# Kernel tuning notes

Hardware: AMD Instinct MI355X
Metric: run time of the kernel (lower is better)

## Reference

```python
import jax, jax.numpy as jnp
import numpy as np

B, C, H, Wd = 4, 64, 64, 64


def setup_inputs() -> dict:
    key = jax.random.key(0)
    k1, k2, k3 = jax.random.split(key, 3)
    x = jax.random.normal(k1, (B, C, H, Wd), dtype=jnp.float32)
    W = jax.random.normal(k2, (C, C), dtype=jnp.float32) * (1.0 / np.sqrt(C))
    b = jax.random.normal(k3, (C,), dtype=jnp.float32) * 0.01
    return {"x": x, "W": W, "b": b}


def reference(x, W, b):
    Bz, Cz, Hz, Wz = x.shape
    N = Hz * Wz
    xf = x.reshape(Bz, Cz, N)                      # values [B,C,N]
    # shared 1x1 conv for queries and keys (same module instance in torch)
    qk = jnp.einsum('oc,bcn->bon', W, xf) + b[None, :, None]  # [B,C,N]
    # scores[b,n,m] = sum_c q[b,c,n] * k[b,c,m], scaled by 1/N
    scores = jnp.einsum('bcn,bcm->bnm', qk, qk) / N           # [B,N,N]
    attn = jax.nn.softmax(scores, axis=-1)                    # softmax over m
    # out[b,c,n] = sum_m values[b,c,m] * attn[b,n,m]
    out = jnp.einsum('bcm,bnm->bcn', xf, attn)
    return out.reshape(Bz, Cz, Hz, Wz)
```

## Files before the change

kernel.cpp:

```cpp
#include <hip/hip_runtime.h>
#include <hip/hip_bf16.h>

#define BATCH 4
#define NSP   4096

#define QKSCALE 0.0187675376f

typedef __bf16 bf16x8v __attribute__((ext_vector_type(8)));
typedef __bf16 bf16x4v __attribute__((ext_vector_type(4)));
typedef float  floatx4 __attribute__((ext_vector_type(4)));
typedef float  floatx16 __attribute__((ext_vector_type(16)));
typedef unsigned uivec2 __attribute__((ext_vector_type(2)));

static __device__ __forceinline__ float fast_exp2(float x) {
#if __has_builtin(__builtin_amdgcn_exp2f)
    return __builtin_amdgcn_exp2f(x);
#else
    return exp2f(x);
#endif
}

static __device__ __forceinline__ unsigned pkbf(float a, float b) {
    union { __bf16 h[2]; unsigned u; } x;
    x.h[0] = (__bf16)a; x.h[1] = (__bf16)b;
    return x.u;
}

static __device__ __forceinline__ void plswap(unsigned &a, unsigned &b) {
#if __has_builtin(__builtin_amdgcn_permlane32_swap)
    uivec2 r = __builtin_amdgcn_permlane32_swap(a, b, false, false);
    a = r[0]; b = r[1];
#else
    asm("v_permlane32_swap_b32 %0, %1" : "+v"(a), "+v"(b));
#endif
}

__global__ __launch_bounds__(256) void qk_kernel(const float* __restrict__ x,
                                                 const float* __restrict__ Wm,
                                                 const float* __restrict__ bias,
                                                 __bf16* __restrict__ qkT,
                                                 __bf16* __restrict__ xbf) {
    __shared__ __align__(16) __bf16 xT[64 * 72];

    const int t  = threadIdx.x;
    const int b  = blockIdx.x >> 6;
    const int n0 = (blockIdx.x & 63) << 6;

#pragma unroll
    for (int p = 0; p < 4; ++p) {
        const int c  = p * 16 + (t >> 4);
        const int n4 = (t & 15) * 4;
        const float4 v = *(const float4*)(x + (size_t)(b * 64 + c) * 4096 + n0 + n4);
        xT[(n4 + 0) * 72 + c] = (__bf16)(v.x * QKSCALE);
        xT[(n4 + 1) * 72 + c] = (__bf16)(v.y * QKSCALE);
        xT[(n4 + 2) * 72 + c] = (__bf16)(v.z * QKSCALE);
        xT[(n4 + 3) * 72 + c] = (__bf16)(v.w * QKSCALE);
        bf16x4v xv;
        xv[0] = (__bf16)v.x; xv[1] = (__bf16)v.y; xv[2] = (__bf16)v.z; xv[3] = (__bf16)v.w;
        *(bf16x4v*)(xbf + (size_t)(b * 64 + c) * 4096 + n0 + n4) = xv;
    }
    __syncthreads();

    const int w = t >> 6, lane = t & 63, quad = lane >> 4, l16 = lane & 15;
    const bf16x8v a0 = *(const bf16x8v*)(xT + (w * 16 + l16) * 72 + quad * 8);
    const bf16x8v a1 = *(const bf16x8v*)(xT + (w * 16 + l16) * 72 + 32 + quad * 8);

    floatx4 acc[4];
#pragma unroll
    for (int ot = 0; ot < 4; ++ot) {
        const float* wr = Wm + (ot * 16 + l16) * 64;
        float4 wa = *(const float4*)(wr + quad * 8);
        float4 wb = *(const float4*)(wr + quad * 8 + 4);
        float4 wc = *(const float4*)(wr + 32 + quad * 8);
        float4 wd = *(const float4*)(wr + 32 + quad * 8 + 4);
        bf16x8v b0, b1;
        b0[0]=(__bf16)wa.x; b0[1]=(__bf16)wa.y; b0[2]=(__bf16)wa.z; b0[3]=(__bf16)wa.w;
        b0[4]=(__bf16)wb.x; b0[5]=(__bf16)wb.y; b0[6]=(__bf16)wb.z; b0[7]=(__bf16)wb.w;
        b1[0]=(__bf16)wc.x; b1[1]=(__bf16)wc.y; b1[2]=(__bf16)wc.z; b1[3]=(__bf16)wc.w;
        b1[4]=(__bf16)wd.x; b1[5]=(__bf16)wd.y; b1[6]=(__bf16)wd.z; b1[7]=(__bf16)wd.w;
        acc[ot] = floatx4{0.f, 0.f, 0.f, 0.f};
        acc[ot] = __builtin_amdgcn_mfma_f32_16x16x32_bf16(a0, b0, acc[ot], 0, 0, 0);
        acc[ot] = __builtin_amdgcn_mfma_f32_16x16x32_bf16(a1, b1, acc[ot], 0, 0, 0);
    }
    __syncthreads();

#pragma unroll
    for (int ot = 0; ot < 4; ++ot) {
        const float bo = bias[ot * 16 + l16] * QKSCALE;
#pragma unroll
        for (int r = 0; r < 4; ++r)
            xT[(w * 16 + quad * 4 + r) * 72 + ot * 16 + l16] = (__bf16)(acc[ot][r] + bo);
    }
    __syncthreads();

    const int n = t >> 2, seg = t & 3;
    __bf16* dst = qkT + (size_t)(b * 4096 + n0 + n) * 64 + seg * 16;
    *(bf16x8v*)dst       = *(const bf16x8v*)(xT + n * 72 + seg * 16);
    *(bf16x8v*)(dst + 8) = *(const bf16x8v*)(xT + n * 72 + seg * 16 + 8);
}

template<int SPLIT, int ITERS>
__global__ __launch_bounds__(512, 4) void attn_kernel(const __bf16* __restrict__ xbf,
                                                      const __bf16* __restrict__ qkT,
                                                      __bf16* __restrict__ Opart,
                                                      float* __restrict__ Lpart) {
    __shared__ __align__(16) char smem[66560];
    __bf16* Klds = (__bf16*)smem;
    __bf16* Vlds = (__bf16*)(smem + 16384);
    float*  Olds = (float*)smem;

    const int t   = threadIdx.x;
    const int blk = blockIdx.x;
    const int xcd = blk & 7;
    const int b   = xcd >> 1;
    const int sub = ((blk >> 3) << 1) | (xcd & 1);
    const int qt  = sub / SPLIT;
    const int s   = sub % SPLIT;
    const int n0  = qt << 8;
    const int pblk = (b * 16 + qt) * SPLIT + s;

    const int w = t >> 6, lane = t & 63, l31 = lane & 31, hi = lane >> 5;

    const __bf16* kgl = qkT + (size_t)b * 4096 * 64;
    const __bf16* vgl = xbf + (size_t)b * 64 * 4096;

    bf16x8v qf[4];
    {
        const __bf16* qrow = kgl + (size_t)(n0 + w * 32 + l31) * 64;
#pragma unroll
        for (int kb = 0; kb < 4; ++kb)
            qf[kb] = *(const bf16x8v*)(qrow + kb * 16 + hi * 8);
    }

    floatx16 oacc[2] = {};
    float rs = 0.f;

    const int srow = t >> 3;
    const int scol = t & 7;
    const int slot = ((scol ^ (srow & 7)) * 8);
    uint4 kst, vst;
    auto stage_load = [&](int m0) {
        kst = *(const uint4*)(kgl + (size_t)(m0 + srow) * 64 + scol * 8);
        vst = *(const uint4*)(vgl + (size_t)srow * 4096 + m0 + scol * 8);
    };
    auto stage_write = [&](int buf) {
        *(uint4*)(Klds + buf * 4096 + srow * 64 + slot) = kst;
        *(uint4*)(Vlds + buf * 4096 + srow * 64 + slot) = vst;
    };

    const int mbase = s * (64 * ITERS);
    stage_load(mbase);
    stage_write(0);
    int cur = 0;

    for (int it = 0; it < ITERS; ++it) {
        if (it + 1 < ITERS) stage_load(mbase + ((it + 1) << 6));
        __syncthreads();
        const __bf16* Kc = Klds + cur * 4096;
        const __bf16* Vc = Vlds + cur * 4096;

        __builtin_amdgcn_s_setprio(1);
#pragma unroll
        for (int mt = 0; mt < 2; ++mt) {
            bf16x8v kf[4];
#pragma unroll
            for (int kb = 0; kb < 4; ++kb)
                kf[kb] = *(const bf16x8v*)(Kc + (mt * 32 + l31) * 64 +
                                           (((kb * 2 + hi) ^ (l31 & 7)) * 8));

            bf16x8v vf[2][2];
#pragma unroll
            for (int ct = 0; ct < 2; ++ct)
#pragma unroll
                for (int ks = 0; ks < 2; ++ks)
                    vf[ct][ks] = *(const bf16x8v*)(Vc + (ct * 32 + l31) * 64 +
                                                   (((mt * 4 + ks * 2 + hi) ^ (l31 & 7)) * 8));

            floatx16 acc = {};
#pragma unroll
            for (int kb = 0; kb < 4; ++kb)
                acc = __builtin_amdgcn_mfma_f32_32x32x16_bf16(kf[kb], qf[kb], acc, 0, 0, 0);

            float p[16];
            float sum = 0.f;
#pragma unroll
            for (int i = 0; i < 16; ++i) { p[i] = fast_exp2(acc[i]); sum += p[i]; }
            rs += sum;

            unsigned wd0 = pkbf(p[0],  p[1]),  wd1 = pkbf(p[2],  p[3]);
            unsigned wd2 = pkbf(p[4],  p[5]),  wd3 = pkbf(p[6],  p[7]);
            unsigned wd4 = pkbf(p[8],  p[9]),  wd5 = pkbf(p[10], p[11]);
            unsigned wd6 = pkbf(p[12], p[13]), wd7 = pkbf(p[14], p[15]);
            plswap(wd0, wd2);
            plswap(wd1, wd3);
            plswap(wd4, wd6);
            plswap(wd5, wd7);
            union { unsigned u[4]; bf16x8v v; } pb0, pb1;
            pb0.u[0] = wd0; pb0.u[1] = wd1; pb0.u[2] = wd2; pb0.u[3] = wd3;
            pb1.u[0] = wd4; pb1.u[1] = wd5; pb1.u[2] = wd6; pb1.u[3] = wd7;

#pragma unroll
            for (int ct = 0; ct < 2; ++ct) {
                oacc[ct] = __builtin_amdgcn_mfma_f32_32x32x16_bf16(vf[ct][0], pb0.v, oacc[ct], 0, 0, 0);
                oacc[ct] = __builtin_amdgcn_mfma_f32_32x32x16_bf16(vf[ct][1], pb1.v, oacc[ct], 0, 0, 0);
            }
        }
        __builtin_amdgcn_s_setprio(0);

        if (it + 1 < ITERS) stage_write(cur ^ 1);
        cur ^= 1;
    }

    {
        float v = rs + __shfl_xor(rs, 32, 64);
        if (lane < 32)
            Lpart[(size_t)pblk * 256 + w * 32 + l31] = v;
    }

    __syncthreads();

#pragma unroll
    for (int ct = 0; ct < 2; ++ct)
#pragma unroll
        for (int r = 0; r < 16; ++r) {
            const int c = ct * 32 + (r & 3) + 8 * (r >> 2) + 4 * hi;
            Olds[c * 260 + w * 32 + l31] = oacc[ct][r];
        }
    __syncthreads();

    const int c = t >> 3, qs = (t & 7) * 32;
#pragma unroll
    for (int i = 0; i < 4; ++i) {
        floatx4 v0 = *(const floatx4*)(Olds + c * 260 + qs + i * 8);
        floatx4 v1 = *(const floatx4*)(Olds + c * 260 + qs + i * 8 + 4);
        bf16x8v pk;
        pk[0]=(__bf16)v0[0]; pk[1]=(__bf16)v0[1]; pk[2]=(__bf16)v0[2]; pk[3]=(__bf16)v0[3];
        pk[4]=(__bf16)v1[0]; pk[5]=(__bf16)v1[1]; pk[6]=(__bf16)v1[2]; pk[7]=(__bf16)v1[3];
        *(bf16x8v*)(Opart + (size_t)pblk * 16384 + c * 256 + qs + i * 8) = pk;
    }
}

template<int SPLIT>
__global__ __launch_bounds__(256) void reduce_kernel(const __bf16* __restrict__ Opart,
                                                     const float* __restrict__ Lpart,
                                                     float* __restrict__ out) {
    const int blk = blockIdx.x;
    const int bq = blk >> 3, cq = blk & 7;
    const int b = bq >> 4, qt = bq & 15;
    const int t = threadIdx.x;
    const int c  = cq * 8 + (t >> 5);
    const int q8 = (t & 31) * 8;

    float l[8] = {0.f,0.f,0.f,0.f,0.f,0.f,0.f,0.f};
#pragma unroll
    for (int s = 0; s < SPLIT; ++s) {
        const float* lp = Lpart + ((size_t)bq * SPLIT + s) * 256 + q8;
        float4 u = *(const float4*)lp;
        float4 v = *(const float4*)(lp + 4);
        l[0]+=u.x; l[1]+=u.y; l[2]+=u.z; l[3]+=u.w;
        l[4]+=v.x; l[5]+=v.y; l[6]+=v.z; l[7]+=v.w;
    }
    float a[8] = {0.f,0.f,0.f,0.f,0.f,0.f,0.f,0.f};
#pragma unroll
    for (int s = 0; s < SPLIT; ++s) {
        bf16x8v v = *(const bf16x8v*)(Opart + ((size_t)bq * SPLIT + s) * 16384 + c * 256 + q8);
#pragma unroll
        for (int k = 0; k < 8; ++k) a[k] += (float)v[k];
    }
    float* op = out + (size_t)(b * 64 + c) * 4096 + qt * 256 + q8;
    float4 o0, o1;
    o0.x = a[0]/l[0]; o0.y = a[1]/l[1]; o0.z = a[2]/l[2]; o0.w = a[3]/l[3];
    o1.x = a[4]/l[4]; o1.y = a[5]/l[5]; o1.z = a[6]/l[6]; o1.w = a[7]/l[7];
    *(float4*)op       = o0;
    *(float4*)(op + 4) = o1;
}

extern "C" void kernel_launch(void* const* d_in, const int* in_sizes, int n_in,
                              void* d_out, int out_size, void* d_ws, size_t ws_size,
                              hipStream_t stream) {
    const float* x    = (const float*)d_in[0];
    const float* Wm   = (const float*)d_in[1];
    const float* bias = (const float*)d_in[2];
    float* out = (float*)d_out;

    char* ws = (char*)d_ws;
    __bf16* qkT = (__bf16*)ws;
    __bf16* xbf = (__bf16*)(ws + 2097152);

    qk_kernel<<<BATCH * (NSP / 64), 256, 0, stream>>>(x, Wm, bias, qkT, xbf);

    const size_t HEAD = 2097152 + 2097152;
    const size_t needBig = HEAD + (size_t)512 * 16384 * 2 + (size_t)512 * 256 * 4;
    if (ws_size >= needBig) {
        __bf16* Opart = (__bf16*)(ws + HEAD);
        float*  Lpart = (float*)(ws + HEAD + (size_t)512 * 16384 * 2);
        attn_kernel<8, 8><<<BATCH * 16 * 8, 512, 0, stream>>>(xbf, qkT, Opart, Lpart);
        reduce_kernel<8><<<512, 256, 0, stream>>>(Opart, Lpart, out);
    } else {
        __bf16* Opart = (__bf16*)(ws + HEAD);
        float*  Lpart = (float*)(ws + HEAD + (size_t)256 * 16384 * 2);
        attn_kernel<4, 16><<<BATCH * 16 * 4, 512, 0, stream>>>(xbf, qkT, Opart, Lpart);
        reduce_kernel<4><<<512, 256, 0, stream>>>(Opart, Lpart, out);
    }
}
```

Baseline: 96.33 us.

## Fuse split-K reduction into attention kernel via last-block atomic counter

Measured after the change: 160.6 us. 1.67x slower.

```diff
diff --git a/kernel.cpp b/kernel.cpp
--- a/kernel.cpp
+++ b/kernel.cpp
@@ -39,12 +39,15 @@
                                                  const float* __restrict__ Wm,
                                                  const float* __restrict__ bias,
                                                  __bf16* __restrict__ qkT,
-                                                 __bf16* __restrict__ xbf) {
+                                                 __bf16* __restrict__ xbf,
+                                                 int* __restrict__ cnt) {
     __shared__ __align__(16) __bf16 xT[64 * 72];
 
     const int t  = threadIdx.x;
     const int b  = blockIdx.x >> 6;
     const int n0 = (blockIdx.x & 63) << 6;
+
+    if (blockIdx.x == 0 && t < 64) cnt[t] = 0;
 
 #pragma unroll
     for (int p = 0; p < 4; ++p) {
@@ -103,7 +106,9 @@
 __global__ __launch_bounds__(512, 4) void attn_kernel(const __bf16* __restrict__ xbf,
                                                       const __bf16* __restrict__ qkT,
                                                       __bf16* __restrict__ Opart,
-                                                      float* __restrict__ Lpart) {
+                                                      float* __restrict__ Lpart,
+                                                      int* __restrict__ cnt,
+                                                      float* __restrict__ out) {
     __shared__ __align__(16) char smem[66560];
     __bf16* Klds = (__bf16*)smem;
     __bf16* Vlds = (__bf16*)(smem + 16384);
@@ -117,7 +122,8 @@
     const int qt  = sub / SPLIT;
     const int s   = sub % SPLIT;
     const int n0  = qt << 8;
-    const int pblk = (b * 16 + qt) * SPLIT + s;
+    const int bq   = b * 16 + qt;
+    const int pblk = bq * SPLIT + s;
 
     const int w = t >> 6, lane = t & 63, l31 = lane & 31, hi = lane >> 5;
 
@@ -228,51 +234,58 @@
         }
     __syncthreads();
 
-    const int c = t >> 3, qs = (t & 7) * 32;
-#pragma unroll
-    for (int i = 0; i < 4; ++i) {
-        floatx4 v0 = *(const floatx4*)(Olds + c * 260 + qs + i * 8);
-        floatx4 v1 = *(const floatx4*)(Olds + c * 260 + qs + i * 8 + 4);
-        bf16x8v pk;
-        pk[0]=(__bf16)v0[0]; pk[1]=(__bf16)v0[1]; pk[2]=(__bf16)v0[2]; pk[3]=(__bf16)v0[3];
-        pk[4]=(__bf16)v1[0]; pk[5]=(__bf16)v1[1]; pk[6]=(__bf16)v1[2]; pk[7]=(__bf16)v1[3];
-        *(bf16x8v*)(Opart + (size_t)pblk * 16384 + c * 256 + qs + i * 8) = pk;
-    }
-}
-
-template<int SPLIT>
-__global__ __launch_bounds__(256) void reduce_kernel(const __bf16* __restrict__ Opart,
-                                                     const float* __restrict__ Lpart,
-                                                     float* __restrict__ out) {
-    const int blk = blockIdx.x;
-    const int bq = blk >> 3, cq = blk & 7;
-    const int b = bq >> 4, qt = bq & 15;
-    const int t = threadIdx.x;
-    const int c  = cq * 8 + (t >> 5);
-    const int q8 = (t & 31) * 8;
-
-    float l[8] = {0.f,0.f,0.f,0.f,0.f,0.f,0.f,0.f};
-#pragma unroll
-    for (int s = 0; s < SPLIT; ++s) {
-        const float* lp = Lpart + ((size_t)bq * SPLIT + s) * 256 + q8;
-        float4 u = *(const float4*)lp;
-        float4 v = *(const float4*)(lp + 4);
-        l[0]+=u.x; l[1]+=u.y; l[2]+=u.z; l[3]+=u.w;
-        l[4]+=v.x; l[5]+=v.y; l[6]+=v.z; l[7]+=v.w;
-    }
-    float a[8] = {0.f,0.f,0.f,0.f,0.f,0.f,0.f,0.f};
-#pragma unroll
-    for (int s = 0; s < SPLIT; ++s) {
-        bf16x8v v = *(const bf16x8v*)(Opart + ((size_t)bq * SPLIT + s) * 16384 + c * 256 + q8);
-#pragma unroll
-        for (int k = 0; k < 8; ++k) a[k] += (float)v[k];
-    }
-    float* op = out + (size_t)(b * 64 + c) * 4096 + qt * 256 + q8;
-    float4 o0, o1;
-    o0.x = a[0]/l[0]; o0.y = a[1]/l[1]; o0.z = a[2]/l[2]; o0.w = a[3]/l[3];
-    o1.x = a[4]/l[4]; o1.y = a[5]/l[5]; o1.z = a[6]/l[6]; o1.w = a[7]/l[7];
-    *(float4*)op       = o0;
-    *(float4*)(op + 4) = o1;
+    {
+        const int c = t >> 3, qs = (t & 7) * 32;
+#pragma unroll
+        for (int i = 0; i < 4; ++i) {
+            floatx4 v0 = *(const floatx4*)(Olds + c * 260 + qs + i * 8);
+            floatx4 v1 = *(const floatx4*)(Olds + c * 260 + qs + i * 8 + 4);
+            bf16x8v pk;
+            pk[0]=(__bf16)v0[0]; pk[1]=(__bf16)v0[1]; pk[2]=(__bf16)v0[2]; pk[3]=(__bf16)v0[3];
+            pk[4]=(__bf16)v1[0]; pk[5]=(__bf16)v1[1]; pk[6]=(__bf16)v1[2]; pk[7]=(__bf16)v1[3];
+            *(bf16x8v*)(Opart + (size_t)pblk * 16384 + c * 256 + qs + i * 8) = pk;
+        }
+    }
+
+    __shared__ int isLast;
+    __syncthreads();
+    if (t == 0) {
+        __threadfence();
+        int old = atomicAdd(cnt + bq, 1);
+        isLast = (old == SPLIT - 1);
+    }
+    __syncthreads();
+    if (!isLast) return;
+    __threadfence();
+
+    float* rl = (float*)smem;
+    if (t < 256) {
+        float sum = 0.f;
+#pragma unroll
+        for (int s2 = 0; s2 < SPLIT; ++s2)
+            sum += Lpart[((size_t)bq * SPLIT + s2) * 256 + t];
+        rl[t] = 1.0f / sum;
+    }
+    __syncthreads();
+
+    const int c = t >> 3, q0 = (t & 7) * 32;
+#pragma unroll
+    for (int j = 0; j < 4; ++j) {
+        const int q8 = q0 + j * 8;
+        float a[8] = {0.f,0.f,0.f,0.f,0.f,0.f,0.f,0.f};
+#pragma unroll
+        for (int s2 = 0; s2 < SPLIT; ++s2) {
+            bf16x8v v = *(const bf16x8v*)(Opart + ((size_t)bq * SPLIT + s2) * 16384 + c * 256 + q8);
+#pragma unroll
+            for (int k = 0; k < 8; ++k) a[k] += (float)v[k];
+        }
+        float* op = out + (size_t)(b * 64 + c) * 4096 + qt * 256 + q8;
+        float4 o0, o1;
+        o0.x = a[0]*rl[q8+0]; o0.y = a[1]*rl[q8+1]; o0.z = a[2]*rl[q8+2]; o0.w = a[3]*rl[q8+3];
+        o1.x = a[4]*rl[q8+4]; o1.y = a[5]*rl[q8+5]; o1.z = a[6]*rl[q8+6]; o1.w = a[7]*rl[q8+7];
+        *(float4*)op       = o0;
+        *(float4*)(op + 4) = o1;
+    }
 }
 
 extern "C" void kernel_launch(void* const* d_in, const int* in_sizes, int n_in,
@@ -286,20 +299,20 @@
     char* ws = (char*)d_ws;
     __bf16* qkT = (__bf16*)ws;
     __bf16* xbf = (__bf16*)(ws + 2097152);
-
-    qk_kernel<<<BATCH * (NSP / 64), 256, 0, stream>>>(x, Wm, bias, qkT, xbf);
-
     const size_t HEAD = 2097152 + 2097152;
-    const size_t needBig = HEAD + (size_t)512 * 16384 * 2 + (size_t)512 * 256 * 4;
+
+    const size_t needBig = HEAD + (size_t)512 * 16384 * 2 + (size_t)512 * 256 * 4 + 256;
     if (ws_size >= needBig) {
         __bf16* Opart = (__bf16*)(ws + HEAD);
         float*  Lpart = (float*)(ws + HEAD + (size_t)512 * 16384 * 2);
-        attn_kernel<8, 8><<<BATCH * 16 * 8, 512, 0, stream>>>(xbf, qkT, Opart, Lpart);
-        reduce_kernel<8><<<512, 256, 0, stream>>>(Opart, Lpart, out);
+        int*    cnt   = (int*)(ws + HEAD + (size_t)512 * 16384 * 2 + (size_t)512 * 256 * 4);
+        qk_kernel<<<BATCH * (NSP / 64), 256, 0, stream>>>(x, Wm, bias, qkT, xbf, cnt);
+        attn_kernel<8, 8><<<BATCH * 16 * 8, 512, 0, stream>>>(xbf, qkT, Opart, Lpart, cnt, out);
     } else {
         __bf16* Opart = (__bf16*)(ws + HEAD);
         float*  Lpart = (float*)(ws + HEAD + (size_t)256 * 16384 * 2);
-        attn_kernel<4, 16><<<BATCH * 16 * 4, 512, 0, stream>>>(xbf, qkT, Opart, Lpart);
-        reduce_kernel<4><<<512, 256, 0, stream>>>(Opart, Lpart, out);
-    }
-}
+        int*    cnt   = (int*)(ws + HEAD + (size_t)256 * 16384 * 2 + (size_t)256 * 256 * 4);
+        qk_kernel<<<BATCH * (NSP / 64), 256, 0, stream>>>(x, Wm, bias, qkT, xbf, cnt);
+        attn_kernel<4, 16><<<BATCH * 16 * 4, 512, 0, stream>>>(xbf, qkT, Opart, Lpart, cnt, out);
+    }
+}
```
